# Optimization experiments

Hardware: AMD Instinct MI355X
Metric: run time of the kernel (lower is better)

Reference implementation:

```python
import jax, jax.numpy as jnp
import numpy as np
from jax import lax

EPS = 1e-5


def _feature_map(t):
    # squared-ReLU feature map + L2 normalize over channel dim (torch F.normalize dim=1)
    t = jax.nn.relu(t) + EPS
    t = t * t
    n = jnp.sqrt(jnp.sum(t * t, axis=1, keepdims=True))
    return t / jnp.maximum(n, 1e-12)


def _forward(x, qkv_w, qkv_b, dwc_w, dwc_b, norm_w, proj_w, proj_b):
    B, C, H, W = x.shape
    N = H * W
    d = norm_w.shape[0]
    # qkv: 1x1 conv (ConvNorm with BN folded into weight/bias)
    qkv = jnp.einsum('bchw,oc->bohw', x, qkv_w) + qkv_b[None, :, None, None]
    qkv = qkv.reshape(B, 3 * d, N)
    q, k, v = jnp.split(qkv, 3, axis=1)  # each [B, d, N]
    q = _feature_map(q)
    k = _feature_map(k)
    # linear-attention associativity path (N > d): attn = (v @ kT) @ q / z
    scale = N ** (-0.5)  # kT.shape[-2] == N
    kmean = jnp.mean(k, axis=2)                       # kT.mean(-2) -> [B, d]
    z = jnp.einsum('bd,bdn->bn', kmean, q)[:, None, :] + EPS  # [B,1,N]
    vkT = jnp.einsum('bin,bjn->bij', v * scale, k * scale)    # [B,d,d]
    attn = jnp.einsum('bij,bjn->bin', vkT, q) / z             # [B,d,N]
    # attn_norm: RMSNorm over channel dim with learnable per-channel weight
    rms = jnp.sqrt(jnp.mean(attn * attn, axis=1, keepdims=True) + EPS)
    attn = attn / rms * norm_w[None, :, None]
    attn = attn.reshape(B, d, H, W)
    # depthwise conv branch on v (RepConv folded to single depthwise conv)
    v_img = v.reshape(B, d, H, W)
    dw = lax.conv_general_dilated(
        v_img, dwc_w, window_strides=(1, 1), padding='SAME',
        feature_group_count=d,
        dimension_numbers=('NCHW', 'OIHW', 'NCHW'))
    dw = dw + dwc_b[None, :, None, None]
    y = attn + dw
    # proj: 1x1 conv d -> dim
    return jnp.einsum('bdhw,cd->bchw', y, proj_w) + proj_b[None, :, None, None]


def setup_inputs() -> dict:
    key = jax.random.key(0)
    ks = jax.random.split(key, 5)
    B, C, H, W = 16, 256, 64, 64
    d, kk = 256, 5
    x = jax.random.normal(ks[0], (B, C, H, W), jnp.float32)
    qkv_w = jax.random.normal(ks[1], (3 * d, C), jnp.float32) * 0.02
    qkv_b = jnp.zeros((3 * d,), jnp.float32)
    dwc_w = jax.random.normal(ks[2], (d, 1, kk, kk), jnp.float32) * 0.02
    dwc_b = jnp.zeros((d,), jnp.float32)
    norm_w = jnp.ones((d,), jnp.float32)
    proj_w = jax.random.normal(ks[3], (C, d), jnp.float32) * 0.02
    proj_b = jnp.zeros((C,), jnp.float32)
    return {'x': x, 'qkv_w': qkv_w, 'qkv_b': qkv_b, 'dwc_w': dwc_w,
            'dwc_b': dwc_b, 'norm_w': norm_w, 'proj_w': proj_w, 'proj_b': proj_b}


def reference(x, qkv_w, qkv_b, dwc_w, dwc_b, norm_w, proj_w, proj_b):
    return _forward(x, qkv_w, qkv_b, dwc_w, dwc_b, norm_w, proj_w, proj_b)
```

## Files before the change

### kernel.cpp

```cpp
#include <hip/hip_runtime.h>
#include <math.h>
#include <stdint.h>

#define FLA_EPS 1e-5f

constexpr int kB  = 16;
constexpr int kD  = 256;
constexpr int kN  = 4096;
constexpr int kO3 = 768;

typedef __attribute__((ext_vector_type(8))) short bf16x8;
typedef __attribute__((ext_vector_type(4))) float f32x4;

__device__ __forceinline__ unsigned short f2bf(float f) {
  union { float f; uint32_t u; } v; v.f = f;
  uint32_t r = v.u + 0x7FFFu + ((v.u >> 16) & 1u);
  return (unsigned short)(r >> 16);
}
__device__ __forceinline__ float bf2f(unsigned short h) {
  union { uint32_t u; float f; } v; v.u = ((uint32_t)h) << 16; return v.f;
}
__device__ __forceinline__ void gl_lds16(const void* g, void* l) {
  __builtin_amdgcn_global_load_lds(
      (const __attribute__((address_space(1))) uint32_t*)g,
      (__attribute__((address_space(3))) uint32_t*)l, 16, 0, 0);
}

__global__ __launch_bounds__(256) void convert_w(
    const float* __restrict__ w, unsigned short* __restrict__ wb, int n) {
  const int i = blockIdx.x * 256 + threadIdx.x;
  if (i < n) wb[i] = f2bf(w[i]);
}

__global__ __launch_bounds__(256) void transpose_x2(
    const float* __restrict__ x, unsigned short* __restrict__ xt) {
  __shared__ float t[64][65];
  const int tid = threadIdx.x;
  const int n0 = blockIdx.x * 64, c0 = blockIdx.y * 64, b = blockIdx.z;
  const float* xb = x + ((long)b * kD + c0) * kN + n0;
#pragma unroll
  for (int r = 0; r < 4; ++r) {
    const int idx = tid + r * 256;
    const int c = idx >> 4, n4 = (idx & 15) * 4;
    const float4 v = *(const float4*)(xb + (long)c * kN + n4);
    t[c][n4] = v.x; t[c][n4 + 1] = v.y; t[c][n4 + 2] = v.z; t[c][n4 + 3] = v.w;
  }
  __syncthreads();
  unsigned short* xtb = xt + ((long)b * kN + n0) * kD + c0;
#pragma unroll
  for (int r = 0; r < 4; ++r) {
    const int idx = tid + r * 256;
    const int n = idx >> 4, cg = (idx & 15) * 4;
    ushort4 o;
    o.x = f2bf(t[cg + 0][n]); o.y = f2bf(t[cg + 1][n]);
    o.z = f2bf(t[cg + 2][n]); o.w = f2bf(t[cg + 3][n]);
    *(ushort4*)&xtb[(long)n * kD + cg] = o;
  }
}

__global__ __launch_bounds__(256) void qkv3_mfma(
    const unsigned short* __restrict__ Wb, const unsigned short* __restrict__ xt,
    const float* __restrict__ bias, unsigned short* __restrict__ qt,
    unsigned short* __restrict__ kb, unsigned short* __restrict__ vb) {
  __shared__ unsigned short sA[256 * 32] __attribute__((aligned(16)));
  __shared__ unsigned short sB[64 * 32] __attribute__((aligned(16)));
  __shared__ float sBias[256];
  __shared__ float colbuf[4][64];
  const int tid = threadIdx.x;
  const int n0 = blockIdx.x * 64, type = blockIdx.y, b = blockIdx.z;
  const int m0 = type * 256;
  const unsigned short* xtb = xt + (long)b * kN * kD;
  const int lane = tid & 63, w = tid >> 6;
  const int lr = lane & 15, lq = lane >> 4;
  sBias[tid] = bias[m0 + tid];

  f32x4 acc[4][4];
#pragma unroll
  for (int i = 0; i < 4; ++i)
#pragma unroll
    for (int j = 0; j < 4; ++j) acc[i][j] = (f32x4){0.f, 0.f, 0.f, 0.f};

  for (int k0 = 0; k0 < 256; k0 += 32) {
#pragma unroll
    for (int r = 0; r < 4; ++r) {
      const int c = tid + r * 256;
      gl_lds16(Wb + (long)(m0 + (c >> 2)) * 256 + k0 + (c & 3) * 8, &sA[c * 8]);
    }
    {
      const int c = tid;
      gl_lds16(xtb + (long)(n0 + (c >> 2)) * 256 + k0 + (c & 3) * 8, &sB[c * 8]);
    }
    __syncthreads();
    bf16x8 af[4], bf[4];
#pragma unroll
    for (int mt = 0; mt < 4; ++mt)
      af[mt] = *(const bf16x8*)&sA[(w * 64 + mt * 16 + lr) * 32 + lq * 8];
#pragma unroll
    for (int nt = 0; nt < 4; ++nt)
      bf[nt] = *(const bf16x8*)&sB[(nt * 16 + lr) * 32 + lq * 8];
#pragma unroll
    for (int mt = 0; mt < 4; ++mt)
#pragma unroll
      for (int nt = 0; nt < 4; ++nt)
        acc[mt][nt] = __builtin_amdgcn_mfma_f32_16x16x32_bf16(
            af[mt], bf[nt], acc[mt][nt], 0, 0, 0);
    __syncthreads();
  }

  if (type < 2) {
    float part[4] = {0.f, 0.f, 0.f, 0.f};
#pragma unroll
    for (int mt = 0; mt < 4; ++mt) {
#pragma unroll
      for (int rr = 0; rr < 4; ++rr) {
        const float bv = sBias[w * 64 + mt * 16 + lq * 4 + rr];
#pragma unroll
        for (int nt = 0; nt < 4; ++nt) {
          const float r_ = fmaxf(acc[mt][nt][rr] + bv, 0.f) + FLA_EPS;
          const float t = r_ * r_;
          acc[mt][nt][rr] = t;
          part[nt] += t * t;
        }
      }
    }
#pragma unroll
    for (int nt = 0; nt < 4; ++nt) {
      part[nt] += __shfl_xor(part[nt], 16);
      part[nt] += __shfl_xor(part[nt], 32);
    }
    if (lq == 0)
#pragma unroll
      for (int nt = 0; nt < 4; ++nt) colbuf[w][nt * 16 + lr] = part[nt];
    __syncthreads();
    float inv[4];
#pragma unroll
    for (int nt = 0; nt < 4; ++nt) {
      const int col = nt * 16 + lr;
      const float S = colbuf[0][col] + colbuf[1][col] + colbuf[2][col] + colbuf[3][col];
      inv[nt] = 1.f / fmaxf(sqrtf(S), 1e-12f);
    }
    if (type == 0) {
      unsigned short* qtb = qt + (long)b * kN * kD;
#pragma unroll
      for (int mt = 0; mt < 4; ++mt)
#pragma unroll
        for (int nt = 0; nt < 4; ++nt) {
          ushort4 o;
          o.x = f2bf(acc[mt][nt][0] * inv[nt]);
          o.y = f2bf(acc[mt][nt][1] * inv[nt]);
          o.z = f2bf(acc[mt][nt][2] * inv[nt]);
          o.w = f2bf(acc[mt][nt][3] * inv[nt]);
          *(ushort4*)&qtb[(long)(n0 + nt * 16 + lr) * kD + w * 64 + mt * 16 + lq * 4] = o;
        }
    } else {
      unsigned short* kbb = kb + (long)b * kD * kN;
#pragma unroll
      for (int mt = 0; mt < 4; ++mt)
#pragma unroll
        for (int rr = 0; rr < 4; ++rr) {
          const int ch = w * 64 + mt * 16 + lq * 4 + rr;
#pragma unroll
          for (int nt = 0; nt < 4; ++nt)
            kbb[(long)ch * kN + n0 + nt * 16 + lr] = f2bf(acc[mt][nt][rr] * inv[nt]);
        }
    }
  } else {
    unsigned short* vbb = vb + (long)b * kD * kN;
#pragma unroll
    for (int mt = 0; mt < 4; ++mt)
#pragma unroll
      for (int rr = 0; rr < 4; ++rr) {
        const int ch = w * 64 + mt * 16 + lq * 4 + rr;
        const float bv = sBias[ch];
#pragma unroll
        for (int nt = 0; nt < 4; ++nt)
          vbb[(long)ch * kN + n0 + nt * 16 + lr] = f2bf(acc[mt][nt][rr] + bv);
      }
  }
}

__global__ __launch_bounds__(256) void kmean2(
    const unsigned short* __restrict__ kb, float* __restrict__ km) {
  const int c = blockIdx.x, b = blockIdx.y;
  const unsigned short* row = kb + ((long)b * kD + c) * kN;
  const int base = threadIdx.x * 16;
  float s = 0.f;
#pragma unroll
  for (int h = 0; h < 2; ++h) {
    uint4 u = *(const uint4*)(row + base + h * 8);
    const unsigned short* p = (const unsigned short*)&u;
#pragma unroll
    for (int i = 0; i < 8; ++i) s += bf2f(p[i]);
  }
#pragma unroll
  for (int m = 1; m < 64; m <<= 1) s += __shfl_xor(s, m);
  __shared__ float red[4];
  if ((threadIdx.x & 63) == 0) red[threadIdx.x >> 6] = s;
  __syncthreads();
  if (threadIdx.x == 0)
    km[b * kD + c] = (red[0] + red[1] + red[2] + red[3]) * (1.f / kN);
}

__global__ __launch_bounds__(256) void vkt2_mfma(
    const unsigned short* __restrict__ vb, const unsigned short* __restrict__ kb,
    float* __restrict__ Tpart) {
  __shared__ unsigned short sA[128 * 32] __attribute__((aligned(16)));
  __shared__ unsigned short sB[128 * 32] __attribute__((aligned(16)));
  const int tid = threadIdx.x;
  const int i0 = blockIdx.x * 128, j0 = blockIdx.y * 128;
  const int b = blockIdx.z >> 3, s = blockIdx.z & 7;
  const unsigned short* vbb = vb + (long)b * kD * kN;
  const unsigned short* kbb = kb + (long)b * kD * kN;
  const int lane = tid & 63, w = tid >> 6;
  const int wm = (w & 1) * 64, wn = (w >> 1) * 64;
  const int lr = lane & 15, lq = lane >> 4;
  const int c0 = tid, c1 = 256 + tid;
  const int am0 = c0 >> 2, ak0 = (c0 & 3) * 8;
  const int am1 = c1 >> 2, ak1 = (c1 & 3) * 8;

  f32x4 acc[4][4];
#pragma unroll
  for (int i = 0; i < 4; ++i)
#pragma unroll
    for (int j = 0; j < 4; ++j) acc[i][j] = (f32x4){0.f, 0.f, 0.f, 0.f};

  for (int n0 = s * 512; n0 < s * 512 + 512; n0 += 32) {
    gl_lds16(vbb + (long)(i0 + am0) * kN + n0 + ak0, &sA[c0 * 8]);
    gl_lds16(vbb + (long)(i0 + am1) * kN + n0 + ak1, &sA[c1 * 8]);
    gl_lds16(kbb + (long)(j0 + am0) * kN + n0 + ak0, &sB[c0 * 8]);
    gl_lds16(kbb + (long)(j0 + am1) * kN + n0 + ak1, &sB[c1 * 8]);
    __syncthreads();
    bf16x8 af[4], bf[4];
#pragma unroll
    for (int mt = 0; mt < 4; ++mt)
      af[mt] = *(const bf16x8*)&sA[(wm + mt * 16 + lr) * 32 + lq * 8];
#pragma unroll
    for (int nt = 0; nt < 4; ++nt)
      bf[nt] = *(const bf16x8*)&sB[(wn + nt * 16 + lr) * 32 + lq * 8];
#pragma unroll
    for (int mt = 0; mt < 4; ++mt)
#pragma unroll
      for (int nt = 0; nt < 4; ++nt)
        acc[mt][nt] = __builtin_amdgcn_mfma_f32_16x16x32_bf16(
            af[mt], bf[nt], acc[mt][nt], 0, 0, 0);
    __syncthreads();
  }
  float* Tp = Tpart + ((long)s * kB + b) * kD * kD;
#pragma unroll
  for (int mt = 0; mt < 4; ++mt)
#pragma unroll
    for (int nt = 0; nt < 4; ++nt) {
      const int j = j0 + wn + nt * 16 + lr;
#pragma unroll
      for (int r = 0; r < 4; ++r) {
        const int i = i0 + wm + mt * 16 + lq * 4 + r;
        Tp[(long)i * kD + j] = acc[mt][nt][r];
      }
    }
}

__global__ __launch_bounds__(256) void tconvert(
    const float* __restrict__ Tpart, unsigned short* __restrict__ Tt) {
  const long idx = (long)blockIdx.x * 256 + threadIdx.x;
  float s = 0.f;
#pragma unroll
  for (int p = 0; p < 8; ++p) s += Tpart[(long)p * 1048576 + idx];
  Tt[idx] = f2bf(s * (1.f / 4096.f));
}

__global__ __launch_bounds__(256) void dwconv3(
    const unsigned short* __restrict__ vb, const float* __restrict__ dwc_w,
    const float* __restrict__ dwc_b, unsigned short* __restrict__ dwp) {
  __shared__ float tile[68][80];
  __shared__ float wt[32];
  const int c = blockIdx.x, b = blockIdx.y;
  const int tid = threadIdx.x;
  if (tid < 25) wt[tid] = dwc_w[c * 25 + tid];
  {
    const float4 z4 = {0.f, 0.f, 0.f, 0.f};
    float* tf = &tile[0][0];
#pragma unroll
    for (int r = 0; r < 6; ++r) {
      const int i = tid + r * 256;
      if (i < 1360) *(float4*)(tf + i * 4) = z4;
    }
  }
  __syncthreads();
  const unsigned short* vp = vb + ((long)b * kD + c) * kN;
#pragma unroll
  for (int r = 0; r < 2; ++r) {
    const int ch = tid + r * 256;
    const int row = ch >> 3, sub = ch & 7;
    const uint4 u = *(const uint4*)(vp + row * 64 + sub * 8);
    const unsigned short* p = (const unsigned short*)&u;
    float4 f0, f1;
    f0.x = bf2f(p[0]); f0.y = bf2f(p[1]); f0.z = bf2f(p[2]); f0.w = bf2f(p[3]);
    f1.x = bf2f(p[4]); f1.y = bf2f(p[5]); f1.z = bf2f(p[6]); f1.w = bf2f(p[7]);
    *(float4*)&tile[row + 2][4 + sub * 8] = f0;
    *(float4*)&tile[row + 2][8 + sub * 8] = f1;
  }
  __syncthreads();
  float w_[25];
#pragma unroll
  for (int i = 0; i < 25; ++i) w_[i] = wt[i];
  const float bias = dwc_b[c];
  const int pr = tid >> 4, pc = tid & 15;
  const int oy0 = pr * 4, ox0 = pc * 4;
  float win[8][12];
#pragma unroll
  for (int r = 0; r < 8; ++r) {
    *(float4*)&win[r][0] = *(const float4*)&tile[oy0 + r][ox0 + 0];
    *(float4*)&win[r][4] = *(const float4*)&tile[oy0 + r][ox0 + 4];
    *(float4*)&win[r][8] = *(const float4*)&tile[oy0 + r][ox0 + 8];
  }
  unsigned short* yp = dwp + ((long)b * kD + c) * kN;
#pragma unroll
  for (int dy = 0; dy < 4; ++dy) {
    ushort4 o;
    unsigned short* op = (unsigned short*)&o;
#pragma unroll
    for (int dx = 0; dx < 4; ++dx) {
      float s = bias;
#pragma unroll
      for (int ky = 0; ky < 5; ++ky)
#pragma unroll
        for (int kx = 0; kx < 5; ++kx)
          s += win[dy + ky][dx + kx + 2] * w_[ky * 5 + kx];
      op[dx] = f2bf(s);
    }
    *(ushort4*)&yp[(oy0 + dy) * 64 + ox0] = o;
  }
}

__global__ __launch_bounds__(256) void attn2_mfma(
    const unsigned short* __restrict__ qt, const unsigned short* __restrict__ Tt,
    const float* __restrict__ kmean, const float* __restrict__ norm_w,
    const unsigned short* __restrict__ dwp, unsigned short* __restrict__ yt) {
  __shared__ unsigned char smem[36864] __attribute__((aligned(16)));
  __shared__ float sKm[256];
  __shared__ float sNw[256];
  __shared__ float zbuf[64];
  __shared__ float rbuf[4][64];
  unsigned short* sQ = (unsigned short*)smem;
  unsigned short* sT = (unsigned short*)(smem + 4096);
  unsigned short* sDw = (unsigned short*)smem;
  const int tid = threadIdx.x;
  const int n0 = blockIdx.x * 64, b = blockIdx.y;
  const unsigned short* qtb = qt + (long)b * kN * kD;
  const unsigned short* Ttb = Tt + (long)b * kD * kD;
  sKm[tid] = kmean[b * kD + tid];
  sNw[tid] = norm_w[tid];
  const int lane = tid & 63, w = tid >> 6;
  const int lr = lane & 15, lq = lane >> 4;

  f32x4 acc[4][4];
#pragma unroll
  for (int i = 0; i < 4; ++i)
#pragma unroll
    for (int j = 0; j < 4; ++j) acc[i][j] = (f32x4){0.f, 0.f, 0.f, 0.f};
  float zp[4] = {0.f, 0.f, 0.f, 0.f};

  for (int k0 = 0; k0 < 256; k0 += 32) {
    {
      const int c = tid;
      gl_lds16(qtb + (long)(n0 + (c >> 2)) * kD + k0 + (c & 3) * 8, &sQ[c * 8]);
    }
#pragma unroll
    for (int r = 0; r < 4; ++r) {
      const int c = tid + r * 256;
      gl_lds16(Ttb + (long)(c >> 2) * kD + k0 + (c & 3) * 8, &sT[c * 8]);
    }
    __syncthreads();
    bf16x8 af[4], bf[4];
#pragma unroll
    for (int mt = 0; mt < 4; ++mt)
      af[mt] = *(const bf16x8*)&sQ[(mt * 16 + lr) * 32 + lq * 8];
#pragma unroll
    for (int nt = 0; nt < 4; ++nt)
      bf[nt] = *(const bf16x8*)&sT[(w * 64 + nt * 16 + lr) * 32 + lq * 8];
#pragma unroll
    for (int mt = 0; mt < 4; ++mt)
#pragma unroll
      for (int j = 0; j < 8; ++j)
        zp[mt] += bf2f((unsigned short)af[mt][j]) * sKm[k0 + lq * 8 + j];
#pragma unroll
    for (int mt = 0; mt < 4; ++mt)
#pragma unroll
      for (int nt = 0; nt < 4; ++nt)
        acc[mt][nt] = __builtin_amdgcn_mfma_f32_16x16x32_bf16(
            af[mt], bf[nt], acc[mt][nt], 0, 0, 0);
    __syncthreads();
  }

  const unsigned short* dwpb = dwp + (long)b * kD * kN;
#pragma unroll
  for (int it = 0; it < 8; ++it) {
    const int c = tid + it * 256;
    const int row = c >> 3, sub = c & 7;
    uint4 t4 = *(const uint4*)(dwpb + (long)row * kN + n0 + sub * 8);
    *(uint4*)&sDw[row * 72 + sub * 8] = t4;
  }
#pragma unroll
  for (int mt = 0; mt < 4; ++mt) {
    zp[mt] += __shfl_xor(zp[mt], 16);
    zp[mt] += __shfl_xor(zp[mt], 32);
  }
  if (w == 0 && lq == 0)
#pragma unroll
    for (int mt = 0; mt < 4; ++mt) zbuf[mt * 16 + lr] = zp[mt];
  __syncthreads();

  float ss[4][4];
#pragma unroll
  for (int mt = 0; mt < 4; ++mt)
#pragma unroll
    for (int r = 0; r < 4; ++r) {
      const float invz = 1.f / (zbuf[mt * 16 + lq * 4 + r] + FLA_EPS);
      float s = 0.f;
#pragma unroll
      for (int nt = 0; nt < 4; ++nt) {
        acc[mt][nt][r] *= invz;
        s += acc[mt][nt][r] * acc[mt][nt][r];
      }
      ss[mt][r] = s;
    }
#pragma unroll
  for (int mt = 0; mt < 4; ++mt)
#pragma unroll
    for (int r = 0; r < 4; ++r) {
      ss[mt][r] += __shfl_xor(ss[mt][r], 1);
      ss[mt][r] += __shfl_xor(ss[mt][r], 2);
      ss[mt][r] += __shfl_xor(ss[mt][r], 4);
      ss[mt][r] += __shfl_xor(ss[mt][r], 8);
    }
  if (lr == 0)
#pragma unroll
    for (int mt = 0; mt < 4; ++mt)
#pragma unroll
      for (int r = 0; r < 4; ++r) rbuf[w][mt * 16 + lq * 4 + r] = ss[mt][r];
  __syncthreads();

  unsigned short* ytb = yt + (long)b * kN * kD;
  float nw[4];
#pragma unroll
  for (int nt = 0; nt < 4; ++nt) nw[nt] = sNw[w * 64 + nt * 16 + lr];
#pragma unroll
  for (int mt = 0; mt < 4; ++mt)
#pragma unroll
    for (int r = 0; r < 4; ++r) {
      const int p = mt * 16 + lq * 4 + r;
      const float S = rbuf[0][p] + rbuf[1][p] + rbuf[2][p] + rbuf[3][p];
      const float scl = rsqrtf(S * (1.f / 256.f) + FLA_EPS);
#pragma unroll
      for (int nt = 0; nt < 4; ++nt) {
        const int ch = w * 64 + nt * 16 + lr;
        const float dw = bf2f(sDw[ch * 72 + p]);
        const float o = acc[mt][nt][r] * scl * nw[nt] + dw;
        ytb[(long)(n0 + p) * kD + ch] = f2bf(o);
      }
    }
}

__global__ __launch_bounds__(256) void proj2_mfma(
    const unsigned short* __restrict__ Wb, const unsigned short* __restrict__ yt,
    const float* __restrict__ bias, float* __restrict__ out) {
  __shared__ unsigned short sA[128 * 32] __attribute__((aligned(16)));
  __shared__ unsigned short sB[128 * 32] __attribute__((aligned(16)));
  const int tid = threadIdx.x;
  const int n0 = blockIdx.x * 128, m0 = blockIdx.y * 128, b = blockIdx.z;
  const unsigned short* ytb = yt + (long)b * kN * kD;
  const int lane = tid & 63, w = tid >> 6;
  const int wm = (w & 1) * 64, wn = (w >> 1) * 64;
  const int lr = lane & 15, lq = lane >> 4;
  const int c0 = tid, c1 = 256 + tid;
  const int am0 = c0 >> 2, ak0 = (c0 & 3) * 8;
  const int am1 = c1 >> 2, ak1 = (c1 & 3) * 8;

  f32x4 acc[4][4];
#pragma unroll
  for (int i = 0; i < 4; ++i)
#pragma unroll
    for (int j = 0; j < 4; ++j) acc[i][j] = (f32x4){0.f, 0.f, 0.f, 0.f};

  for (int k0 = 0; k0 < 256; k0 += 32) {
    gl_lds16(Wb + (long)(m0 + am0) * kD + k0 + ak0, &sA[c0 * 8]);
    gl_lds16(Wb + (long)(m0 + am1) * kD + k0 + ak1, &sA[c1 * 8]);
    gl_lds16(ytb + (long)(n0 + am0) * kD + k0 + ak0, &sB[c0 * 8]);
    gl_lds16(ytb + (long)(n0 + am1) * kD + k0 + ak1, &sB[c1 * 8]);
    __syncthreads();
    bf16x8 af[4], bf[4];
#pragma unroll
    for (int mt = 0; mt < 4; ++mt)
      af[mt] = *(const bf16x8*)&sA[(wm + mt * 16 + lr) * 32 + lq * 8];
#pragma unroll
    for (int nt = 0; nt < 4; ++nt)
      bf[nt] = *(const bf16x8*)&sB[(wn + nt * 16 + lr) * 32 + lq * 8];
#pragma unroll
    for (int mt = 0; mt < 4; ++mt)
#pragma unroll
      for (int nt = 0; nt < 4; ++nt)
        acc[mt][nt] = __builtin_amdgcn_mfma_f32_16x16x32_bf16(
            af[mt], bf[nt], acc[mt][nt], 0, 0, 0);
    __syncthreads();
  }
  float* ob = out + (long)b * kD * kN;
#pragma unroll
  for (int mt = 0; mt < 4; ++mt)
#pragma unroll
    for (int nt = 0; nt < 4; ++nt) {
      const int n = n0 + wn + nt * 16 + lr;
#pragma unroll
      for (int r = 0; r < 4; ++r) {
        const int m = m0 + wm + mt * 16 + lq * 4 + r;
        ob[(long)m * kN + n] = acc[mt][nt][r] + bias[m];
      }
    }
}

extern "C" void kernel_launch(void* const* d_in, const int* in_sizes, int n_in,
                              void* d_out, int out_size, void* d_ws,
                              size_t ws_size, hipStream_t stream) {
  const float* x      = (const float*)d_in[0];
  const float* qkv_w  = (const float*)d_in[1];
  const float* qkv_b  = (const float*)d_in[2];
  const float* dwc_w  = (const float*)d_in[3];
  const float* dwc_b  = (const float*)d_in[4];
  const float* norm_w = (const float*)d_in[5];
  const float* proj_w = (const float*)d_in[6];
  const float* proj_b = (const float*)d_in[7];
  float* out = (float*)d_out;
  char* ws = (char*)d_ws;

  constexpr long SZ = 33554432;
  unsigned short* qt  = (unsigned short*)(ws);
  unsigned short* kb  = (unsigned short*)(ws + SZ);
  unsigned short* vb  = (unsigned short*)(ws + 2 * SZ);
  unsigned short* dwp = (unsigned short*)(ws + 3 * SZ);
  unsigned short* yt  = (unsigned short*)(ws + 4 * SZ);
  unsigned short* xt  = (unsigned short*)(ws + 5 * SZ);
  float* Tpart        = (float*)(ws + 5 * SZ);
  unsigned short* Tt  = (unsigned short*)(ws + 6 * SZ);
  unsigned short* wqb = (unsigned short*)(ws + 6 * SZ + 2097152);
  unsigned short* wpb = (unsigned short*)(ws + 6 * SZ + 2097152 + 393216);
  float* km           = (float*)(ws + 6 * SZ + 2097152 + 393216 + 131072);

  convert_w<<<768, 256, 0, stream>>>(qkv_w, wqb, kO3 * kD);
  convert_w<<<256, 256, 0, stream>>>(proj_w, wpb, kD * kD);
  transpose_x2<<<dim3(64, 4, 16), 256, 0, stream>>>(x, xt);
  qkv3_mfma<<<dim3(64, 3, 16), 256, 0, stream>>>(wqb, xt, qkv_b, qt, kb, vb);
  kmean2<<<dim3(256, 16), 256, 0, stream>>>(kb, km);
  vkt2_mfma<<<dim3(2, 2, 128), 256, 0, stream>>>(vb, kb, Tpart);
  tconvert<<<4096, 256, 0, stream>>>(Tpart, Tt);
  dwconv3<<<dim3(256, 16), 256, 0, stream>>>(vb, dwc_w, dwc_b, dwp);
  attn2_mfma<<<dim3(64, 16), 256, 0, stream>>>(qt, Tt, km, norm_w, dwp, yt);
  proj2_mfma<<<dim3(32, 2, 16), 256, 0, stream>>>(wpb, yt, proj_b, out);
}
```

Measured before the change: 301.3 us.

## Keep QKV weights in registers, double-buffer swizzled x tiles, fuse k-mean

The QKV projection kernel now loads each wave's 64x256 weight slice into registers once. It loops over four 64-column tiles per block, prefetching the next full-K x tile into a double-buffered, XOR-swizzled LDS buffer. The k-mean reduction is folded into the k epilogue using shuffles and atomicAdd onto a memset buffer, which removes a separate kernel that re-read k. The trade-offs are higher register pressure from the 32 bf16x8 weight fragments, 64KB of LDS per block, a quarter as many blocks, and atomics that make the mean's summation order nondeterministic.

```diff
diff --git a/kernel.cpp b/kernel.cpp
--- a/kernel.cpp
+++ b/kernel.cpp
@@ -58,147 +58,166 @@
   }
 }
 
-__global__ __launch_bounds__(256) void qkv3_mfma(
+__global__ __launch_bounds__(256, 2) void qkv4_mfma(
     const unsigned short* __restrict__ Wb, const unsigned short* __restrict__ xt,
     const float* __restrict__ bias, unsigned short* __restrict__ qt,
-    unsigned short* __restrict__ kb, unsigned short* __restrict__ vb) {
-  __shared__ unsigned short sA[256 * 32] __attribute__((aligned(16)));
-  __shared__ unsigned short sB[64 * 32] __attribute__((aligned(16)));
+    unsigned short* __restrict__ kb, unsigned short* __restrict__ vb,
+    float* __restrict__ km) {
+  __shared__ unsigned short sB[2][64 * 256] __attribute__((aligned(16)));
   __shared__ float sBias[256];
-  __shared__ float colbuf[4][64];
+  __shared__ float colbuf[2][4][64];
   const int tid = threadIdx.x;
-  const int n0 = blockIdx.x * 64, type = blockIdx.y, b = blockIdx.z;
+  const int g = blockIdx.x;
+  const int type = blockIdx.y, b = blockIdx.z;
   const int m0 = type * 256;
   const unsigned short* xtb = xt + (long)b * kN * kD;
   const int lane = tid & 63, w = tid >> 6;
   const int lr = lane & 15, lq = lane >> 4;
   sBias[tid] = bias[m0 + tid];
 
-  f32x4 acc[4][4];
-#pragma unroll
-  for (int i = 0; i < 4; ++i)
-#pragma unroll
-    for (int j = 0; j < 4; ++j) acc[i][j] = (f32x4){0.f, 0.f, 0.f, 0.f};
-
-  for (int k0 = 0; k0 < 256; k0 += 32) {
-#pragma unroll
-    for (int r = 0; r < 4; ++r) {
+  bf16x8 aw[8][4];
+  {
+    const unsigned short* wp = Wb + (long)(m0 + w * 64 + lr) * kD + lq * 8;
+#pragma unroll
+    for (int kk = 0; kk < 8; ++kk)
+#pragma unroll
+      for (int mt = 0; mt < 4; ++mt)
+        aw[kk][mt] = *(const bf16x8*)(wp + (long)(mt * 16) * kD + kk * 32);
+  }
+
+  {
+    const int nb = g * 256;
+#pragma unroll
+    for (int r = 0; r < 8; ++r) {
       const int c = tid + r * 256;
-      gl_lds16(Wb + (long)(m0 + (c >> 2)) * 256 + k0 + (c & 3) * 8, &sA[c * 8]);
-    }
-    {
-      const int c = tid;
-      gl_lds16(xtb + (long)(n0 + (c >> 2)) * 256 + k0 + (c & 3) * 8, &sB[c * 8]);
-    }
-    __syncthreads();
-    bf16x8 af[4], bf[4];
-#pragma unroll
-    for (int mt = 0; mt < 4; ++mt)
-      af[mt] = *(const bf16x8*)&sA[(w * 64 + mt * 16 + lr) * 32 + lq * 8];
-#pragma unroll
-    for (int nt = 0; nt < 4; ++nt)
-      bf[nt] = *(const bf16x8*)&sB[(nt * 16 + lr) * 32 + lq * 8];
-#pragma unroll
-    for (int mt = 0; mt < 4; ++mt)
-#pragma unroll
-      for (int nt = 0; nt < 4; ++nt)
-        acc[mt][nt] = __builtin_amdgcn_mfma_f32_16x16x32_bf16(
-            af[mt], bf[nt], acc[mt][nt], 0, 0, 0);
-    __syncthreads();
-  }
-
-  if (type < 2) {
-    float part[4] = {0.f, 0.f, 0.f, 0.f};
-#pragma unroll
-    for (int mt = 0; mt < 4; ++mt) {
-#pragma unroll
-      for (int rr = 0; rr < 4; ++rr) {
-        const float bv = sBias[w * 64 + mt * 16 + lq * 4 + rr];
-#pragma unroll
-        for (int nt = 0; nt < 4; ++nt) {
-          const float r_ = fmaxf(acc[mt][nt][rr] + bv, 0.f) + FLA_EPS;
-          const float t = r_ * r_;
-          acc[mt][nt][rr] = t;
-          part[nt] += t * t;
+      const int n = c >> 5;
+      const int slot = (c & 31) ^ (n & 7);
+      gl_lds16(xtb + (long)(nb + n) * kD + slot * 8, &sB[0][c * 8]);
+    }
+  }
+  __syncthreads();
+
+  for (int t = 0; t < 4; ++t) {
+    const int n0 = g * 256 + t * 64;
+    const int cur = t & 1;
+    if (t < 3) {
+#pragma unroll
+      for (int r = 0; r < 8; ++r) {
+        const int c = tid + r * 256;
+        const int n = c >> 5;
+        const int slot = (c & 31) ^ (n & 7);
+        gl_lds16(xtb + (long)(n0 + 64 + n) * kD + slot * 8, &sB[cur ^ 1][c * 8]);
+      }
+    }
+
+    f32x4 acc[4][4];
+#pragma unroll
+    for (int i = 0; i < 4; ++i)
+#pragma unroll
+      for (int j = 0; j < 4; ++j) acc[i][j] = (f32x4){0.f, 0.f, 0.f, 0.f};
+
+#pragma unroll
+    for (int kk = 0; kk < 8; ++kk) {
+      bf16x8 bfr[4];
+#pragma unroll
+      for (int nt = 0; nt < 4; ++nt) {
+        const int row = nt * 16 + lr;
+        const int e = (row * 256 + kk * 32 + lq * 8) ^ ((lr & 7) << 3);
+        bfr[nt] = *(const bf16x8*)&sB[cur][e];
+      }
+#pragma unroll
+      for (int mt = 0; mt < 4; ++mt)
+#pragma unroll
+        for (int nt = 0; nt < 4; ++nt)
+          acc[mt][nt] = __builtin_amdgcn_mfma_f32_16x16x32_bf16(
+              aw[kk][mt], bfr[nt], acc[mt][nt], 0, 0, 0);
+    }
+
+    if (type < 2) {
+      float part[4] = {0.f, 0.f, 0.f, 0.f};
+#pragma unroll
+      for (int mt = 0; mt < 4; ++mt) {
+#pragma unroll
+        for (int rr = 0; rr < 4; ++rr) {
+          const float bv = sBias[w * 64 + mt * 16 + lq * 4 + rr];
+#pragma unroll
+          for (int nt = 0; nt < 4; ++nt) {
+            const float r_ = fmaxf(acc[mt][nt][rr] + bv, 0.f) + FLA_EPS;
+            const float tt = r_ * r_;
+            acc[mt][nt][rr] = tt;
+            part[nt] += tt * tt;
+          }
         }
       }
-    }
-#pragma unroll
-    for (int nt = 0; nt < 4; ++nt) {
-      part[nt] += __shfl_xor(part[nt], 16);
-      part[nt] += __shfl_xor(part[nt], 32);
-    }
-    if (lq == 0)
-#pragma unroll
-      for (int nt = 0; nt < 4; ++nt) colbuf[w][nt * 16 + lr] = part[nt];
-    __syncthreads();
-    float inv[4];
-#pragma unroll
-    for (int nt = 0; nt < 4; ++nt) {
-      const int col = nt * 16 + lr;
-      const float S = colbuf[0][col] + colbuf[1][col] + colbuf[2][col] + colbuf[3][col];
-      inv[nt] = 1.f / fmaxf(sqrtf(S), 1e-12f);
-    }
-    if (type == 0) {
-      unsigned short* qtb = qt + (long)b * kN * kD;
-#pragma unroll
-      for (int mt = 0; mt < 4; ++mt)
-#pragma unroll
-        for (int nt = 0; nt < 4; ++nt) {
-          ushort4 o;
-          o.x = f2bf(acc[mt][nt][0] * inv[nt]);
-          o.y = f2bf(acc[mt][nt][1] * inv[nt]);
-          o.z = f2bf(acc[mt][nt][2] * inv[nt]);
-          o.w = f2bf(acc[mt][nt][3] * inv[nt]);
-          *(ushort4*)&qtb[(long)(n0 + nt * 16 + lr) * kD + w * 64 + mt * 16 + lq * 4] = o;
-        }
+#pragma unroll
+      for (int nt = 0; nt < 4; ++nt) {
+        part[nt] += __shfl_xor(part[nt], 16);
+        part[nt] += __shfl_xor(part[nt], 32);
+      }
+      if (lq == 0)
+#pragma unroll
+        for (int nt = 0; nt < 4; ++nt) colbuf[cur][w][nt * 16 + lr] = part[nt];
+    }
+    __syncthreads();
+
+    if (type < 2) {
+      float inv[4];
+#pragma unroll
+      for (int nt = 0; nt < 4; ++nt) {
+        const int col = nt * 16 + lr;
+        const float S = colbuf[cur][0][col] + colbuf[cur][1][col] +
+                        colbuf[cur][2][col] + colbuf[cur][3][col];
+        inv[nt] = 1.f / fmaxf(sqrtf(S), 1e-12f);
+      }
+      if (type == 0) {
+        unsigned short* qtb = qt + (long)b * kN * kD;
+#pragma unroll
+        for (int mt = 0; mt < 4; ++mt)
+#pragma unroll
+          for (int nt = 0; nt < 4; ++nt) {
+            ushort4 o;
+            o.x = f2bf(acc[mt][nt][0] * inv[nt]);
+            o.y = f2bf(acc[mt][nt][1] * inv[nt]);
+            o.z = f2bf(acc[mt][nt][2] * inv[nt]);
+            o.w = f2bf(acc[mt][nt][3] * inv[nt]);
+            *(ushort4*)&qtb[(long)(n0 + nt * 16 + lr) * kD +
+                            w * 64 + mt * 16 + lq * 4] = o;
+          }
+      } else {
+        unsigned short* kbb = kb + (long)b * kD * kN;
+#pragma unroll
+        for (int mt = 0; mt < 4; ++mt)
+#pragma unroll
+          for (int rr = 0; rr < 4; ++rr) {
+            const int ch = w * 64 + mt * 16 + lq * 4 + rr;
+            float ks = 0.f;
+#pragma unroll
+            for (int nt = 0; nt < 4; ++nt) {
+              const unsigned short sv = f2bf(acc[mt][nt][rr] * inv[nt]);
+              kbb[(long)ch * kN + n0 + nt * 16 + lr] = sv;
+              ks += bf2f(sv);
+            }
+            ks += __shfl_xor(ks, 1);
+            ks += __shfl_xor(ks, 2);
+            ks += __shfl_xor(ks, 4);
+            ks += __shfl_xor(ks, 8);
+            if (lr == 0) atomicAdd(&km[b * kD + ch], ks * (1.f / kN));
+          }
+      }
     } else {
-      unsigned short* kbb = kb + (long)b * kD * kN;
+      unsigned short* vbb = vb + (long)b * kD * kN;
 #pragma unroll
       for (int mt = 0; mt < 4; ++mt)
 #pragma unroll
         for (int rr = 0; rr < 4; ++rr) {
           const int ch = w * 64 + mt * 16 + lq * 4 + rr;
+          const float bv = sBias[ch];
 #pragma unroll
           for (int nt = 0; nt < 4; ++nt)
-            kbb[(long)ch * kN + n0 + nt * 16 + lr] = f2bf(acc[mt][nt][rr] * inv[nt]);
+            vbb[(long)ch * kN + n0 + nt * 16 + lr] = f2bf(acc[mt][nt][rr] + bv);
         }
     }
-  } else {
-    unsigned short* vbb = vb + (long)b * kD * kN;
-#pragma unroll
-    for (int mt = 0; mt < 4; ++mt)
-#pragma unroll
-      for (int rr = 0; rr < 4; ++rr) {
-        const int ch = w * 64 + mt * 16 + lq * 4 + rr;
-        const float bv = sBias[ch];
-#pragma unroll
-        for (int nt = 0; nt < 4; ++nt)
-          vbb[(long)ch * kN + n0 + nt * 16 + lr] = f2bf(acc[mt][nt][rr] + bv);
-      }
-  }
-}
-
-__global__ __launch_bounds__(256) void kmean2(
-    const unsigned short* __restrict__ kb, float* __restrict__ km) {
-  const int c = blockIdx.x, b = blockIdx.y;
-  const unsigned short* row = kb + ((long)b * kD + c) * kN;
-  const int base = threadIdx.x * 16;
-  float s = 0.f;
-#pragma unroll
-  for (int h = 0; h < 2; ++h) {
-    uint4 u = *(const uint4*)(row + base + h * 8);
-    const unsigned short* p = (const unsigned short*)&u;
-#pragma unroll
-    for (int i = 0; i < 8; ++i) s += bf2f(p[i]);
-  }
-#pragma unroll
-  for (int m = 1; m < 64; m <<= 1) s += __shfl_xor(s, m);
-  __shared__ float red[4];
-  if ((threadIdx.x & 63) == 0) red[threadIdx.x >> 6] = s;
-  __syncthreads();
-  if (threadIdx.x == 0)
-    km[b * kD + c] = (red[0] + red[1] + red[2] + red[3]) * (1.f / kN);
+  }
 }
 
 __global__ __launch_bounds__(256) void vkt2_mfma(
@@ -547,8 +566,8 @@
   convert_w<<<768, 256, 0, stream>>>(qkv_w, wqb, kO3 * kD);
   convert_w<<<256, 256, 0, stream>>>(proj_w, wpb, kD * kD);
   transpose_x2<<<dim3(64, 4, 16), 256, 0, stream>>>(x, xt);
-  qkv3_mfma<<<dim3(64, 3, 16), 256, 0, stream>>>(wqb, xt, qkv_b, qt, kb, vb);
-  kmean2<<<dim3(256, 16), 256, 0, stream>>>(kb, km);
+  hipMemsetAsync(km, 0, kB * kD * sizeof(float), stream);
+  qkv4_mfma<<<dim3(16, 3, 16), 256, 0, stream>>>(wqb, xt, qkv_b, qt, kb, vb, km);
   vkt2_mfma<<<dim3(2, 2, 128), 256, 0, stream>>>(vb, kb, Tpart);
   tconvert<<<4096, 256, 0, stream>>>(Tpart, Tt);
   dwconv3<<<dim3(256, 16), 256, 0, stream>>>(vb, dwc_w, dwc_b, dwp);
```

Result: slower. 395.4 us (+31.2%).

## Swizzle LDS k-chunks in MFMA GEMMs and fuse key mean into qkv epilogue

Applied to the files above, without the earlier changes.

Applies an XOR swizzle to the source address of 16-byte global-to-LDS chunks and to the matching LDS fragment reads in all four MFMA GEMM kernels, to remove LDS bank conflicts on the 64-byte row stride. It also drops the separate kmean kernel: the qkv epilogue reduces each k channel's bf16 values across lanes and atomically adds them into a zeroed km buffer. This saves one pass over the k tensor and a kernel launch, at the cost of float atomics, which make the summation order nondeterministic, plus an extra memset.

```diff
diff --git a/kernel.cpp b/kernel.cpp
--- a/kernel.cpp
+++ b/kernel.cpp
@@ -25,6 +25,8 @@
       (const __attribute__((address_space(1))) uint32_t*)g,
       (__attribute__((address_space(3))) uint32_t*)l, 16, 0, 0);
 }
+
+#define SWZ_SRC(c) (((c) & 3) ^ (((c) >> 3) & 3))
 
 __global__ __launch_bounds__(256) void convert_w(
     const float* __restrict__ w, unsigned short* __restrict__ wb, int n) {
@@ -58,10 +60,11 @@
   }
 }
 
-__global__ __launch_bounds__(256) void qkv3_mfma(
+__global__ __launch_bounds__(256) void qkv6_mfma(
     const unsigned short* __restrict__ Wb, const unsigned short* __restrict__ xt,
     const float* __restrict__ bias, unsigned short* __restrict__ qt,
-    unsigned short* __restrict__ kb, unsigned short* __restrict__ vb) {
+    unsigned short* __restrict__ kb, unsigned short* __restrict__ vb,
+    float* __restrict__ km) {
   __shared__ unsigned short sA[256 * 32] __attribute__((aligned(16)));
   __shared__ unsigned short sB[64 * 32] __attribute__((aligned(16)));
   __shared__ float sBias[256];
@@ -72,6 +75,7 @@
   const unsigned short* xtb = xt + (long)b * kN * kD;
   const int lane = tid & 63, w = tid >> 6;
   const int lr = lane & 15, lq = lane >> 4;
+  const int sxk = (lq ^ ((lr >> 1) & 3)) * 8;
   sBias[tid] = bias[m0 + tid];
 
   f32x4 acc[4][4];
@@ -84,26 +88,28 @@
 #pragma unroll
     for (int r = 0; r < 4; ++r) {
       const int c = tid + r * 256;
-      gl_lds16(Wb + (long)(m0 + (c >> 2)) * 256 + k0 + (c & 3) * 8, &sA[c * 8]);
+      gl_lds16(Wb + (long)(m0 + (c >> 2)) * 256 + k0 + SWZ_SRC(c) * 8,
+               &sA[c * 8]);
     }
     {
       const int c = tid;
-      gl_lds16(xtb + (long)(n0 + (c >> 2)) * 256 + k0 + (c & 3) * 8, &sB[c * 8]);
-    }
-    __syncthreads();
-    bf16x8 af[4], bf[4];
-#pragma unroll
-    for (int mt = 0; mt < 4; ++mt)
-      af[mt] = *(const bf16x8*)&sA[(w * 64 + mt * 16 + lr) * 32 + lq * 8];
+      gl_lds16(xtb + (long)(n0 + (c >> 2)) * kD + k0 + SWZ_SRC(c) * 8,
+               &sB[c * 8]);
+    }
+    __syncthreads();
+    bf16x8 af[4], bfr[4];
+#pragma unroll
+    for (int mt = 0; mt < 4; ++mt)
+      af[mt] = *(const bf16x8*)&sA[(w * 64 + mt * 16 + lr) * 32 + sxk];
 #pragma unroll
     for (int nt = 0; nt < 4; ++nt)
-      bf[nt] = *(const bf16x8*)&sB[(nt * 16 + lr) * 32 + lq * 8];
+      bfr[nt] = *(const bf16x8*)&sB[(nt * 16 + lr) * 32 + sxk];
 #pragma unroll
     for (int mt = 0; mt < 4; ++mt)
 #pragma unroll
       for (int nt = 0; nt < 4; ++nt)
         acc[mt][nt] = __builtin_amdgcn_mfma_f32_16x16x32_bf16(
-            af[mt], bf[nt], acc[mt][nt], 0, 0, 0);
+            af[mt], bfr[nt], acc[mt][nt], 0, 0, 0);
     __syncthreads();
   }
 
@@ -159,9 +165,18 @@
 #pragma unroll
         for (int rr = 0; rr < 4; ++rr) {
           const int ch = w * 64 + mt * 16 + lq * 4 + rr;
-#pragma unroll
-          for (int nt = 0; nt < 4; ++nt)
-            kbb[(long)ch * kN + n0 + nt * 16 + lr] = f2bf(acc[mt][nt][rr] * inv[nt]);
+          float ks = 0.f;
+#pragma unroll
+          for (int nt = 0; nt < 4; ++nt) {
+            const unsigned short sv = f2bf(acc[mt][nt][rr] * inv[nt]);
+            kbb[(long)ch * kN + n0 + nt * 16 + lr] = sv;
+            ks += bf2f(sv);
+          }
+          ks += __shfl_xor(ks, 1);
+          ks += __shfl_xor(ks, 2);
+          ks += __shfl_xor(ks, 4);
+          ks += __shfl_xor(ks, 8);
+          if (lr == 0) atomicAdd(&km[b * kD + ch], ks * (1.f / kN));
         }
     }
   } else {
@@ -179,29 +194,7 @@
   }
 }
 
-__global__ __launch_bounds__(256) void kmean2(
-    const unsigned short* __restrict__ kb, float* __restrict__ km) {
-  const int c = blockIdx.x, b = blockIdx.y;
-  const unsigned short* row = kb + ((long)b * kD + c) * kN;
-  const int base = threadIdx.x * 16;
-  float s = 0.f;
-#pragma unroll
-  for (int h = 0; h < 2; ++h) {
-    uint4 u = *(const uint4*)(row + base + h * 8);
-    const unsigned short* p = (const unsigned short*)&u;
-#pragma unroll
-    for (int i = 0; i < 8; ++i) s += bf2f(p[i]);
-  }
-#pragma unroll
-  for (int m = 1; m < 64; m <<= 1) s += __shfl_xor(s, m);
-  __shared__ float red[4];
-  if ((threadIdx.x & 63) == 0) red[threadIdx.x >> 6] = s;
-  __syncthreads();
-  if (threadIdx.x == 0)
-    km[b * kD + c] = (red[0] + red[1] + red[2] + red[3]) * (1.f / kN);
-}
-
-__global__ __launch_bounds__(256) void vkt2_mfma(
+__global__ __launch_bounds__(256) void vkt4_mfma(
     const unsigned short* __restrict__ vb, const unsigned short* __restrict__ kb,
     float* __restrict__ Tpart) {
   __shared__ unsigned short sA[128 * 32] __attribute__((aligned(16)));
@@ -214,9 +207,10 @@
   const int lane = tid & 63, w = tid >> 6;
   const int wm = (w & 1) * 64, wn = (w >> 1) * 64;
   const int lr = lane & 15, lq = lane >> 4;
+  const int sxk = (lq ^ ((lr >> 1) & 3)) * 8;
   const int c0 = tid, c1 = 256 + tid;
-  const int am0 = c0 >> 2, ak0 = (c0 & 3) * 8;
-  const int am1 = c1 >> 2, ak1 = (c1 & 3) * 8;
+  const int am0 = c0 >> 2, ak0 = SWZ_SRC(c0) * 8;
+  const int am1 = c1 >> 2, ak1 = SWZ_SRC(c1) * 8;
 
   f32x4 acc[4][4];
 #pragma unroll
@@ -233,10 +227,10 @@
     bf16x8 af[4], bf[4];
 #pragma unroll
     for (int mt = 0; mt < 4; ++mt)
-      af[mt] = *(const bf16x8*)&sA[(wm + mt * 16 + lr) * 32 + lq * 8];
+      af[mt] = *(const bf16x8*)&sA[(wm + mt * 16 + lr) * 32 + sxk];
 #pragma unroll
     for (int nt = 0; nt < 4; ++nt)
-      bf[nt] = *(const bf16x8*)&sB[(wn + nt * 16 + lr) * 32 + lq * 8];
+      bf[nt] = *(const bf16x8*)&sB[(wn + nt * 16 + lr) * 32 + sxk];
 #pragma unroll
     for (int mt = 0; mt < 4; ++mt)
 #pragma unroll
@@ -332,7 +326,7 @@
   }
 }
 
-__global__ __launch_bounds__(256) void attn2_mfma(
+__global__ __launch_bounds__(256) void attn4_mfma(
     const unsigned short* __restrict__ qt, const unsigned short* __restrict__ Tt,
     const float* __restrict__ kmean, const float* __restrict__ norm_w,
     const unsigned short* __restrict__ dwp, unsigned short* __restrict__ yt) {
@@ -352,6 +346,7 @@
   sNw[tid] = norm_w[tid];
   const int lane = tid & 63, w = tid >> 6;
   const int lr = lane & 15, lq = lane >> 4;
+  const int sxk = (lq ^ ((lr >> 1) & 3)) * 8;
 
   f32x4 acc[4][4];
 #pragma unroll
@@ -363,21 +358,22 @@
   for (int k0 = 0; k0 < 256; k0 += 32) {
     {
       const int c = tid;
-      gl_lds16(qtb + (long)(n0 + (c >> 2)) * kD + k0 + (c & 3) * 8, &sQ[c * 8]);
+      gl_lds16(qtb + (long)(n0 + (c >> 2)) * kD + k0 + SWZ_SRC(c) * 8,
+               &sQ[c * 8]);
     }
 #pragma unroll
     for (int r = 0; r < 4; ++r) {
       const int c = tid + r * 256;
-      gl_lds16(Ttb + (long)(c >> 2) * kD + k0 + (c & 3) * 8, &sT[c * 8]);
+      gl_lds16(Ttb + (long)(c >> 2) * kD + k0 + SWZ_SRC(c) * 8, &sT[c * 8]);
     }
     __syncthreads();
     bf16x8 af[4], bf[4];
 #pragma unroll
     for (int mt = 0; mt < 4; ++mt)
-      af[mt] = *(const bf16x8*)&sQ[(mt * 16 + lr) * 32 + lq * 8];
+      af[mt] = *(const bf16x8*)&sQ[(mt * 16 + lr) * 32 + sxk];
 #pragma unroll
     for (int nt = 0; nt < 4; ++nt)
-      bf[nt] = *(const bf16x8*)&sT[(w * 64 + nt * 16 + lr) * 32 + lq * 8];
+      bf[nt] = *(const bf16x8*)&sT[(w * 64 + nt * 16 + lr) * 32 + sxk];
 #pragma unroll
     for (int mt = 0; mt < 4; ++mt)
 #pragma unroll
@@ -461,7 +457,7 @@
     }
 }
 
-__global__ __launch_bounds__(256) void proj2_mfma(
+__global__ __launch_bounds__(256) void proj4_mfma(
     const unsigned short* __restrict__ Wb, const unsigned short* __restrict__ yt,
     const float* __restrict__ bias, float* __restrict__ out) {
   __shared__ unsigned short sA[128 * 32] __attribute__((aligned(16)));
@@ -472,9 +468,10 @@
   const int lane = tid & 63, w = tid >> 6;
   const int wm = (w & 1) * 64, wn = (w >> 1) * 64;
   const int lr = lane & 15, lq = lane >> 4;
+  const int sxk = (lq ^ ((lr >> 1) & 3)) * 8;
   const int c0 = tid, c1 = 256 + tid;
-  const int am0 = c0 >> 2, ak0 = (c0 & 3) * 8;
-  const int am1 = c1 >> 2, ak1 = (c1 & 3) * 8;
+  const int am0 = c0 >> 2, ak0 = SWZ_SRC(c0) * 8;
+  const int am1 = c1 >> 2, ak1 = SWZ_SRC(c1) * 8;
 
   f32x4 acc[4][4];
 #pragma unroll
@@ -491,10 +488,10 @@
     bf16x8 af[4], bf[4];
 #pragma unroll
     for (int mt = 0; mt < 4; ++mt)
-      af[mt] = *(const bf16x8*)&sA[(wm + mt * 16 + lr) * 32 + lq * 8];
+      af[mt] = *(const bf16x8*)&sA[(wm + mt * 16 + lr) * 32 + sxk];
 #pragma unroll
     for (int nt = 0; nt < 4; ++nt)
-      bf[nt] = *(const bf16x8*)&sB[(wn + nt * 16 + lr) * 32 + lq * 8];
+      bf[nt] = *(const bf16x8*)&sB[(wn + nt * 16 + lr) * 32 + sxk];
 #pragma unroll
     for (int mt = 0; mt < 4; ++mt)
 #pragma unroll
@@ -547,11 +544,11 @@
   convert_w<<<768, 256, 0, stream>>>(qkv_w, wqb, kO3 * kD);
   convert_w<<<256, 256, 0, stream>>>(proj_w, wpb, kD * kD);
   transpose_x2<<<dim3(64, 4, 16), 256, 0, stream>>>(x, xt);
-  qkv3_mfma<<<dim3(64, 3, 16), 256, 0, stream>>>(wqb, xt, qkv_b, qt, kb, vb);
-  kmean2<<<dim3(256, 16), 256, 0, stream>>>(kb, km);
-  vkt2_mfma<<<dim3(2, 2, 128), 256, 0, stream>>>(vb, kb, Tpart);
+  hipMemsetAsync(km, 0, kB * kD * sizeof(float), stream);
+  qkv6_mfma<<<dim3(64, 3, 16), 256, 0, stream>>>(wqb, xt, qkv_b, qt, kb, vb, km);
+  vkt4_mfma<<<dim3(2, 2, 128), 256, 0, stream>>>(vb, kb, Tpart);
   tconvert<<<4096, 256, 0, stream>>>(Tpart, Tt);
   dwconv3<<<dim3(256, 16), 256, 0, stream>>>(vb, dwc_w, dwc_b, dwp);
-  attn2_mfma<<<dim3(64, 16), 256, 0, stream>>>(qt, Tt, km, norm_w, dwp, yt);
-  proj2_mfma<<<dim3(32, 2, 16), 256, 0, stream>>>(wpb, yt, proj_b, out);
-}
+  attn4_mfma<<<dim3(64, 16), 256, 0, stream>>>(qt, Tt, km, norm_w, dwp, yt);
+  proj4_mfma<<<dim3(32, 2, 16), 256, 0, stream>>>(wpb, yt, proj_b, out);
+}
```

After: 302.3 us. Within noise of the previous version (+0.3%).

## Fuse k-mean into QKV epilogue and projection into attention kernel

Applied to the files above, without the earlier changes.

The k-mean reduction moves into the QKV GEMM epilogue, using wave shuffles and atomics into a zeroed buffer, which removes the separate kmean kernel and its re-read of k. The 1x1 projection GEMM now runs inside the attention kernel: the y tile stays in LDS and the kernel writes fp32 output directly, so the yt intermediate is never written to or read from global memory. In exchange, LDS use per block grows (an extra ~33KB buffer), which may lower occupancy, and atomics make the k-mean summation order nondeterministic.

```diff
diff --git a/kernel.cpp b/kernel.cpp
--- a/kernel.cpp
+++ b/kernel.cpp
@@ -58,10 +58,11 @@
   }
 }
 
-__global__ __launch_bounds__(256) void qkv3_mfma(
+__global__ __launch_bounds__(256) void qkv7_mfma(
     const unsigned short* __restrict__ Wb, const unsigned short* __restrict__ xt,
     const float* __restrict__ bias, unsigned short* __restrict__ qt,
-    unsigned short* __restrict__ kb, unsigned short* __restrict__ vb) {
+    unsigned short* __restrict__ kb, unsigned short* __restrict__ vb,
+    float* __restrict__ km) {
   __shared__ unsigned short sA[256 * 32] __attribute__((aligned(16)));
   __shared__ unsigned short sB[64 * 32] __attribute__((aligned(16)));
   __shared__ float sBias[256];
@@ -88,22 +89,22 @@
     }
     {
       const int c = tid;
-      gl_lds16(xtb + (long)(n0 + (c >> 2)) * 256 + k0 + (c & 3) * 8, &sB[c * 8]);
-    }
-    __syncthreads();
-    bf16x8 af[4], bf[4];
+      gl_lds16(xtb + (long)(n0 + (c >> 2)) * kD + k0 + (c & 3) * 8, &sB[c * 8]);
+    }
+    __syncthreads();
+    bf16x8 af[4], bfr[4];
 #pragma unroll
     for (int mt = 0; mt < 4; ++mt)
       af[mt] = *(const bf16x8*)&sA[(w * 64 + mt * 16 + lr) * 32 + lq * 8];
 #pragma unroll
     for (int nt = 0; nt < 4; ++nt)
-      bf[nt] = *(const bf16x8*)&sB[(nt * 16 + lr) * 32 + lq * 8];
+      bfr[nt] = *(const bf16x8*)&sB[(nt * 16 + lr) * 32 + lq * 8];
 #pragma unroll
     for (int mt = 0; mt < 4; ++mt)
 #pragma unroll
       for (int nt = 0; nt < 4; ++nt)
         acc[mt][nt] = __builtin_amdgcn_mfma_f32_16x16x32_bf16(
-            af[mt], bf[nt], acc[mt][nt], 0, 0, 0);
+            af[mt], bfr[nt], acc[mt][nt], 0, 0, 0);
     __syncthreads();
   }
 
@@ -159,9 +160,18 @@
 #pragma unroll
         for (int rr = 0; rr < 4; ++rr) {
           const int ch = w * 64 + mt * 16 + lq * 4 + rr;
-#pragma unroll
-          for (int nt = 0; nt < 4; ++nt)
-            kbb[(long)ch * kN + n0 + nt * 16 + lr] = f2bf(acc[mt][nt][rr] * inv[nt]);
+          float ks = 0.f;
+#pragma unroll
+          for (int nt = 0; nt < 4; ++nt) {
+            const unsigned short sv = f2bf(acc[mt][nt][rr] * inv[nt]);
+            kbb[(long)ch * kN + n0 + nt * 16 + lr] = sv;
+            ks += bf2f(sv);
+          }
+          ks += __shfl_xor(ks, 1);
+          ks += __shfl_xor(ks, 2);
+          ks += __shfl_xor(ks, 4);
+          ks += __shfl_xor(ks, 8);
+          if (lr == 0) atomicAdd(&km[b * kD + ch], ks * (1.f / kN));
         }
     }
   } else {
@@ -177,28 +187,6 @@
           vbb[(long)ch * kN + n0 + nt * 16 + lr] = f2bf(acc[mt][nt][rr] + bv);
       }
   }
-}
-
-__global__ __launch_bounds__(256) void kmean2(
-    const unsigned short* __restrict__ kb, float* __restrict__ km) {
-  const int c = blockIdx.x, b = blockIdx.y;
-  const unsigned short* row = kb + ((long)b * kD + c) * kN;
-  const int base = threadIdx.x * 16;
-  float s = 0.f;
-#pragma unroll
-  for (int h = 0; h < 2; ++h) {
-    uint4 u = *(const uint4*)(row + base + h * 8);
-    const unsigned short* p = (const unsigned short*)&u;
-#pragma unroll
-    for (int i = 0; i < 8; ++i) s += bf2f(p[i]);
-  }
-#pragma unroll
-  for (int m = 1; m < 64; m <<= 1) s += __shfl_xor(s, m);
-  __shared__ float red[4];
-  if ((threadIdx.x & 63) == 0) red[threadIdx.x >> 6] = s;
-  __syncthreads();
-  if (threadIdx.x == 0)
-    km[b * kD + c] = (red[0] + red[1] + red[2] + red[3]) * (1.f / kN);
 }
 
 __global__ __launch_bounds__(256) void vkt2_mfma(
@@ -332,11 +320,13 @@
   }
 }
 
-__global__ __launch_bounds__(256) void attn2_mfma(
+__global__ __launch_bounds__(256) void attnproj_mfma(
     const unsigned short* __restrict__ qt, const unsigned short* __restrict__ Tt,
     const float* __restrict__ kmean, const float* __restrict__ norm_w,
-    const unsigned short* __restrict__ dwp, unsigned short* __restrict__ yt) {
+    const unsigned short* __restrict__ dwp, const unsigned short* __restrict__ Pw,
+    const float* __restrict__ proj_b, float* __restrict__ out) {
   __shared__ unsigned char smem[36864] __attribute__((aligned(16)));
+  __shared__ unsigned short sY[64 * 264] __attribute__((aligned(16)));
   __shared__ float sKm[256];
   __shared__ float sNw[256];
   __shared__ float zbuf[64];
@@ -344,6 +334,7 @@
   unsigned short* sQ = (unsigned short*)smem;
   unsigned short* sT = (unsigned short*)(smem + 4096);
   unsigned short* sDw = (unsigned short*)smem;
+  unsigned short* sP = (unsigned short*)smem;
   const int tid = threadIdx.x;
   const int n0 = blockIdx.x * 64, b = blockIdx.y;
   const unsigned short* qtb = qt + (long)b * kN * kD;
@@ -440,7 +431,6 @@
       for (int r = 0; r < 4; ++r) rbuf[w][mt * 16 + lq * 4 + r] = ss[mt][r];
   __syncthreads();
 
-  unsigned short* ytb = yt + (long)b * kN * kD;
   float nw[4];
 #pragma unroll
   for (int nt = 0; nt < 4; ++nt) nw[nt] = sNw[w * 64 + nt * 16 + lr];
@@ -455,65 +445,53 @@
       for (int nt = 0; nt < 4; ++nt) {
         const int ch = w * 64 + nt * 16 + lr;
         const float dw = bf2f(sDw[ch * 72 + p]);
-        const float o = acc[mt][nt][r] * scl * nw[nt] + dw;
-        ytb[(long)(n0 + p) * kD + ch] = f2bf(o);
+        sY[p * 264 + ch] = f2bf(acc[mt][nt][r] * scl * nw[nt] + dw);
       }
     }
-}
-
-__global__ __launch_bounds__(256) void proj2_mfma(
-    const unsigned short* __restrict__ Wb, const unsigned short* __restrict__ yt,
-    const float* __restrict__ bias, float* __restrict__ out) {
-  __shared__ unsigned short sA[128 * 32] __attribute__((aligned(16)));
-  __shared__ unsigned short sB[128 * 32] __attribute__((aligned(16)));
-  const int tid = threadIdx.x;
-  const int n0 = blockIdx.x * 128, m0 = blockIdx.y * 128, b = blockIdx.z;
-  const unsigned short* ytb = yt + (long)b * kN * kD;
-  const int lane = tid & 63, w = tid >> 6;
-  const int wm = (w & 1) * 64, wn = (w >> 1) * 64;
-  const int lr = lane & 15, lq = lane >> 4;
-  const int c0 = tid, c1 = 256 + tid;
-  const int am0 = c0 >> 2, ak0 = (c0 & 3) * 8;
-  const int am1 = c1 >> 2, ak1 = (c1 & 3) * 8;
-
-  f32x4 acc[4][4];
+  __syncthreads();
+
+  f32x4 acc2[4][4];
 #pragma unroll
   for (int i = 0; i < 4; ++i)
 #pragma unroll
-    for (int j = 0; j < 4; ++j) acc[i][j] = (f32x4){0.f, 0.f, 0.f, 0.f};
-
-  for (int k0 = 0; k0 < 256; k0 += 32) {
-    gl_lds16(Wb + (long)(m0 + am0) * kD + k0 + ak0, &sA[c0 * 8]);
-    gl_lds16(Wb + (long)(m0 + am1) * kD + k0 + ak1, &sA[c1 * 8]);
-    gl_lds16(ytb + (long)(n0 + am0) * kD + k0 + ak0, &sB[c0 * 8]);
-    gl_lds16(ytb + (long)(n0 + am1) * kD + k0 + ak1, &sB[c1 * 8]);
+    for (int j = 0; j < 4; ++j) acc2[i][j] = (f32x4){0.f, 0.f, 0.f, 0.f};
+  int bo[4];
+#pragma unroll
+  for (int nt = 0; nt < 4; ++nt) bo[nt] = (nt * 16 + lr) * 264 + lq * 8;
+
+  for (int kk = 0; kk < 8; ++kk) {
+#pragma unroll
+    for (int r = 0; r < 4; ++r) {
+      const int c = tid + r * 256;
+      gl_lds16(Pw + (long)(c >> 2) * 256 + kk * 32 + (c & 3) * 8, &sP[c * 8]);
+    }
     __syncthreads();
     bf16x8 af[4], bf[4];
 #pragma unroll
     for (int mt = 0; mt < 4; ++mt)
-      af[mt] = *(const bf16x8*)&sA[(wm + mt * 16 + lr) * 32 + lq * 8];
+      af[mt] = *(const bf16x8*)&sP[(w * 64 + mt * 16 + lr) * 32 + lq * 8];
 #pragma unroll
     for (int nt = 0; nt < 4; ++nt)
-      bf[nt] = *(const bf16x8*)&sB[(wn + nt * 16 + lr) * 32 + lq * 8];
+      bf[nt] = *(const bf16x8*)&sY[bo[nt] + kk * 32];
 #pragma unroll
     for (int mt = 0; mt < 4; ++mt)
 #pragma unroll
       for (int nt = 0; nt < 4; ++nt)
-        acc[mt][nt] = __builtin_amdgcn_mfma_f32_16x16x32_bf16(
-            af[mt], bf[nt], acc[mt][nt], 0, 0, 0);
-    __syncthreads();
-  }
+        acc2[mt][nt] = __builtin_amdgcn_mfma_f32_16x16x32_bf16(
+            af[mt], bf[nt], acc2[mt][nt], 0, 0, 0);
+    __syncthreads();
+  }
+
   float* ob = out + (long)b * kD * kN;
 #pragma unroll
   for (int mt = 0; mt < 4; ++mt)
 #pragma unroll
-    for (int nt = 0; nt < 4; ++nt) {
-      const int n = n0 + wn + nt * 16 + lr;
-#pragma unroll
-      for (int r = 0; r < 4; ++r) {
-        const int m = m0 + wm + mt * 16 + lq * 4 + r;
-        ob[(long)m * kN + n] = acc[mt][nt][r] + bias[m];
-      }
+    for (int r = 0; r < 4; ++r) {
+      const int m = w * 64 + mt * 16 + lq * 4 + r;
+      const float pb = proj_b[m];
+#pragma unroll
+      for (int nt = 0; nt < 4; ++nt)
+        ob[(long)m * kN + n0 + nt * 16 + lr] = acc2[mt][nt][r] + pb;
     }
 }
 
@@ -536,7 +514,6 @@
   unsigned short* kb  = (unsigned short*)(ws + SZ);
   unsigned short* vb  = (unsigned short*)(ws + 2 * SZ);
   unsigned short* dwp = (unsigned short*)(ws + 3 * SZ);
-  unsigned short* yt  = (unsigned short*)(ws + 4 * SZ);
   unsigned short* xt  = (unsigned short*)(ws + 5 * SZ);
   float* Tpart        = (float*)(ws + 5 * SZ);
   unsigned short* Tt  = (unsigned short*)(ws + 6 * SZ);
@@ -547,11 +524,11 @@
   convert_w<<<768, 256, 0, stream>>>(qkv_w, wqb, kO3 * kD);
   convert_w<<<256, 256, 0, stream>>>(proj_w, wpb, kD * kD);
   transpose_x2<<<dim3(64, 4, 16), 256, 0, stream>>>(x, xt);
-  qkv3_mfma<<<dim3(64, 3, 16), 256, 0, stream>>>(wqb, xt, qkv_b, qt, kb, vb);
-  kmean2<<<dim3(256, 16), 256, 0, stream>>>(kb, km);
+  hipMemsetAsync(km, 0, kB * kD * sizeof(float), stream);
+  qkv7_mfma<<<dim3(64, 3, 16), 256, 0, stream>>>(wqb, xt, qkv_b, qt, kb, vb, km);
   vkt2_mfma<<<dim3(2, 2, 128), 256, 0, stream>>>(vb, kb, Tpart);
   tconvert<<<4096, 256, 0, stream>>>(Tpart, Tt);
   dwconv3<<<dim3(256, 16), 256, 0, stream>>>(vb, dwc_w, dwc_b, dwp);
-  attn2_mfma<<<dim3(64, 16), 256, 0, stream>>>(qt, Tt, km, norm_w, dwp, yt);
-  proj2_mfma<<<dim3(32, 2, 16), 256, 0, stream>>>(wpb, yt, proj_b, out);
-}
+  attnproj_mfma<<<dim3(64, 16), 256, 0, stream>>>(qt, Tt, km, norm_w, dwp,
+                                                  wpb, proj_b, out);
+}
```

Result: faster. 294.5 us (-2.2%).
